# Kernel tuning notes

Measured on AMD Instinct MI355X. Metric: run time of the kernel, lower is better.

Reference implementation:

```python
import jax, jax.numpy as jnp
import numpy as np

B, NKV, NQ, D, H = 4, 2048, 1024, 1024, 16
HD = D // H


def setup_inputs() -> dict:
    key = jax.random.key(0)
    ks = jax.random.split(key, 9)
    s = 0.02
    return {
        "x": jax.random.normal(ks[0], (B, NKV, D), jnp.float32),
        "y": jax.random.normal(ks[1], (B, NQ, D), jnp.float32),
        "mask": jax.random.randint(ks[2], (B, NQ, NKV), 0, 2, jnp.int32),
        "W_kv": jax.random.normal(ks[3], (D, 2 * D), jnp.float32) * s,
        "b_kv": jnp.zeros((2 * D,), jnp.float32),
        "W_q": jax.random.normal(ks[4], (D, D), jnp.float32) * s,
        "b_q": jnp.zeros((D,), jnp.float32),
        "W_o": jax.random.normal(ks[5], (D, D), jnp.float32) * s,
        "b_o": jnp.zeros((D,), jnp.float32),
    }


def reference(x, y, mask, W_kv, b_kv, W_q, b_q, W_o, b_o):
    b, nkv, _ = x.shape
    nq = y.shape[1]
    kv = x @ W_kv + b_kv                                  # [B, NKV, 2D]
    q = y @ W_q + b_q                                     # [B, NQ, D]
    kv = kv.reshape(b, nkv, H, 2 * HD).transpose(0, 2, 1, 3)  # [B,H,NKV,2HD]
    q = q.reshape(b, nq, H, HD).transpose(0, 2, 1, 3)         # [B,H,NQ,HD]
    k, v = kv[..., :HD], kv[..., HD:]
    scores = jnp.einsum('bhqd,bhkd->bhqk', q, k) / jnp.sqrt(jnp.float32(HD))
    scores = jnp.where(mask[:, None, :, :] == 0, jnp.float32(-1e20), scores)
    attn = jax.nn.softmax(scores, axis=-1)
    vals = jnp.einsum('bhqk,bhkd->bhqd', attn, v)          # [B,H,NQ,HD]
    vals = vals.transpose(0, 2, 1, 3).reshape(b, nq, D)
    return vals @ W_o + b_o
```

## Files before the change

### kernel.cpp

```cpp
#include <hip/hip_runtime.h>
#include <hip/hip_bf16.h>
#include <math.h>

#define B_   4
#define NKV_ 2048
#define NQ_  1024
#define D_   1024
#define H_   16
#define HD_  64

typedef __attribute__((ext_vector_type(8))) short bf16x8;
typedef __attribute__((ext_vector_type(4))) float f32x4;

#define MFMA16x32(a, b, c) __builtin_amdgcn_mfma_f32_16x16x32_bf16((a), (b), (c), 0, 0, 0)

#define SC_LOG2 0.1803368801111244f

__device__ __forceinline__ short f2bf(float f) {
    unsigned u = __builtin_bit_cast(unsigned, f);
    u = (u + 0x7fff + ((u >> 16) & 1)) >> 16;
    return (short)u;
}
__device__ __forceinline__ unsigned cvt_pk_bf16(float lo, float hi) {
    unsigned r;
    asm("v_cvt_pk_bf16_f32 %0, %1, %2" : "=v"(r) : "v"(lo), "v"(hi));
    return r;
}
__device__ __forceinline__ void gload_lds16(const void* g, void* l) {
    __builtin_amdgcn_global_load_lds(
        (const __attribute__((address_space(1))) void*)g,
        (__attribute__((address_space(3))) void*)l, 16, 0, 0);
}
__device__ __forceinline__ void barrier_raw() {
    asm volatile("" ::: "memory");
    __builtin_amdgcn_s_barrier();
    asm volatile("" ::: "memory");
}

__global__ __launch_bounds__(256)
void prep(const float* __restrict__ Wkv, short* __restrict__ Tkv,
          const float* __restrict__ Wq,  short* __restrict__ Tq,
          const float* __restrict__ Wo,  short* __restrict__ To,
          const int* __restrict__ mask,  unsigned short* __restrict__ m16,
          const float* __restrict__ x,   short* __restrict__ xh, int n4x,
          const float* __restrict__ y,   short* __restrict__ yh, int n4y)
{
    const int bid = (int)blockIdx.x;
    if (bid < 4096) {
        const float* W; short* T; int K, N, bx, by;
        if (bid < 2048)      { W = Wkv; T = Tkv; K = D_; N = 2 * D_; bx = bid & 63;          by = bid >> 6; }
        else if (bid < 3072) { W = Wq;  T = Tq;  K = D_; N = D_;     bx = (bid - 2048) & 31; by = (bid - 2048) >> 5; }
        else                 { W = Wo;  T = To;  K = D_; N = D_;     bx = (bid - 3072) & 31; by = (bid - 3072) >> 5; }
        __shared__ float tile[32][33];
        const int tx = threadIdx.x & 31, ty = threadIdx.x >> 5;
        const int n0 = bx * 32, k0 = by * 32;
#pragma unroll
        for (int i = 0; i < 4; ++i)
            tile[ty + 8 * i][tx] = W[(size_t)(k0 + ty + 8 * i) * N + n0 + tx];
        __syncthreads();
#pragma unroll
        for (int i = 0; i < 4; ++i)
            T[(size_t)(n0 + ty + 8 * i) * K + k0 + tx] = f2bf(tile[tx][ty + 8 * i]);
    } else if (bid < 4608) {
        const int w = (bid - 4096) * 256 + threadIdx.x;
        const int4* pp = reinterpret_cast<const int4*>(mask + (size_t)w * 64);
        unsigned wg0 = 0, wg1 = 0, wg2 = 0, wg3 = 0;
#pragma unroll
        for (int i = 0; i < 16; ++i) {
            const int4 v = pp[i];
            const unsigned nib = (unsigned)(v.x != 0) | ((unsigned)(v.y != 0) << 1)
                               | ((unsigned)(v.z != 0) << 2) | ((unsigned)(v.w != 0) << 3);
            const unsigned sh = 4u * (unsigned)(i >> 2);
            if ((i & 3) == 0) wg0 |= nib << sh;
            else if ((i & 3) == 1) wg1 |= nib << sh;
            else if ((i & 3) == 2) wg2 |= nib << sh;
            else wg3 |= nib << sh;
        }
        ushort4 o;
        o.x = (unsigned short)wg0; o.y = (unsigned short)wg1;
        o.z = (unsigned short)wg2; o.w = (unsigned short)wg3;
        reinterpret_cast<ushort4*>(m16)[w] = o;
    } else {
        const int ntot = n4x + n4y;
        for (int i = (bid - 4608) * 256 + threadIdx.x; i < ntot; i += 2048 * 256) {
            const float4 v = (i < n4x)
                ? reinterpret_cast<const float4*>(x)[i]
                : reinterpret_cast<const float4*>(y)[i - n4x];
            short4 h;
            h.x = f2bf(v.x); h.y = f2bf(v.y); h.z = f2bf(v.z); h.w = f2bf(v.w);
            if (i < n4x) reinterpret_cast<short4*>(xh)[i] = h;
            else         reinterpret_cast<short4*>(yh)[i - n4x] = h;
        }
    }
}

__global__ __launch_bounds__(512, 2)
void proj256(const short* __restrict__ A, const short* __restrict__ Bm,
             const float* __restrict__ bias, short* __restrict__ Kout,
             short* __restrict__ Vtout)
{
    constexpr int K  = 1024;
    constexpr int NT = K / 32;
    constexpr int M  = B_ * NKV_;
    constexpr int N  = 2 * D_;

    __shared__ short At[4][8192];
    __shared__ short Bt[4][8192];

    const int t    = threadIdx.x;
    const int wave = t >> 6;
    const int lane = t & 63;
    const int fr   = lane & 15;
    const int kq   = lane >> 4;
    const int wm0  = (wave >> 2) * 128;
    const int wn0  = (wave & 3) * 64;

    const int gx  = N >> 8;
    const int gy  = M >> 8;
    const int lgx = __builtin_ctz(gx);
    const int bid = (int)blockIdx.x;
    const int xcd = bid & 7;
    const int j   = bid >> 3;
    const int m0  = (xcd * (gy >> 3) + (j >> lgx)) * 256;
    const int n0  = (j & (gx - 1)) * 256;

    const int r1 = t >> 2;
    const int g1 = (t & 3) ^ ((r1 >> 1) & 3);
    const int r2 = r1 + 128;

    f32x4 acc[8][4];
#pragma unroll
    for (int i = 0; i < 8; ++i)
#pragma unroll
        for (int j2 = 0; j2 < 4; ++j2) acc[i][j2] = f32x4{0.f, 0.f, 0.f, 0.f};

    auto stage = [&](int sb, int it) {
        const int kk = it << 5;
        gload_lds16(A  + (size_t)(m0 + r1) * K + kk + 8 * g1, &At[sb][wave * 512]);
        gload_lds16(A  + (size_t)(m0 + r2) * K + kk + 8 * g1, &At[sb][4096 + wave * 512]);
        gload_lds16(Bm + (size_t)(n0 + r1) * K + kk + 8 * g1, &Bt[sb][wave * 512]);
        gload_lds16(Bm + (size_t)(n0 + r2) * K + kk + 8 * g1, &Bt[sb][4096 + wave * 512]);
    };

    stage(0, 0);
    stage(1, 1);
    stage(2, 2);

    const int gsw = ((kq ^ ((fr >> 1) & 3)) << 3);
    for (int it = 0; it < NT; ++it) {
        if (it < NT - 2)       asm volatile("s_waitcnt vmcnt(8)" ::: "memory");
        else if (it == NT - 2) asm volatile("s_waitcnt vmcnt(4)" ::: "memory");
        else                   asm volatile("s_waitcnt vmcnt(0)" ::: "memory");
        barrier_raw();

        const int cb = it & 3;
        bf16x8 af[8], bf[4];
#pragma unroll
        for (int i = 0; i < 8; ++i)
            af[i] = *reinterpret_cast<const bf16x8*>(
                &At[cb][(wm0 + i * 16 + fr) * 32 + gsw]);
#pragma unroll
        for (int i = 0; i < 4; ++i)
            bf[i] = *reinterpret_cast<const bf16x8*>(
                &Bt[cb][(wn0 + i * 16 + fr) * 32 + gsw]);

        if (it + 3 < NT) stage((it + 3) & 3, it + 3);

        __builtin_amdgcn_s_setprio(1);
#pragma unroll
        for (int i = 0; i < 8; ++i)
#pragma unroll
            for (int j2 = 0; j2 < 4; ++j2)
                acc[i][j2] = MFMA16x32(af[i], bf[j2], acc[i][j2]);
        __builtin_amdgcn_s_setprio(0);
    }

#pragma unroll
    for (int i = 0; i < 8; ++i) {
#pragma unroll
        for (int j2 = 0; j2 < 4; ++j2) {
#pragma unroll
            for (int r = 0; r < 4; ++r) {
                const int m = m0 + wm0 + i * 16 + (lane >> 4) * 4 + r;
                const int n = n0 + wn0 + j2 * 16 + fr;
                const float v = acc[i][j2][r] + bias[n];
                const int b  = m >> 11;
                const int nk = m & 2047;
                const int h  = n >> 7;
                const int c  = n & 127;
                const int bh = b * H_ + h;
                if (c < 64)
                    Kout[(((size_t)bh * NKV_ + nk) << 6) + c] = f2bf(v);
                else
                    Vtout[((size_t)bh * 64 + (c - 64)) * NKV_ + nk] = f2bf(v);
            }
        }
    }
}

template<int MODE>
__global__ __launch_bounds__(256)
void gemm64(const short* __restrict__ Ahi, const short* __restrict__ Bhi,
            const float* __restrict__ bias, void* __restrict__ outv)
{
    __shared__ short At[3][2048];
    __shared__ short Bt[3][4096];

    const int M = B_ * NQ_, N = D_, K = D_;
    const int t    = threadIdx.x;
    const int wave = t >> 6;
    const int lane = t & 63;
    const int fr   = lane & 15;
    const int kq   = lane >> 4;

    const int gx  = N >> 7;
    const int gy  = M >> 6;
    const int lgx = __builtin_ctz(gx);
    const int bid = (int)blockIdx.x;
    const int xcd = bid & 7;
    const int j   = bid >> 3;
    const int m0  = (xcd * (gy >> 3) + (j >> lgx)) * 64;
    const int n0  = (j & (gx - 1)) * 128;

    const int wm0 = (wave & 1) * 32;
    const int wn0 = (wave >> 1) * 64;
    const int NT  = K >> 5;

    const int rA = t >> 2, gA = (t & 3) ^ ((rA >> 1) & 3);
    const int r1 = t >> 2,         g1 = (t & 3) ^ ((r1 >> 1) & 3);
    const int r2 = (t + 256) >> 2, g2 = (t & 3) ^ ((r2 >> 1) & 3);

    f32x4 acc[2][4];
#pragma unroll
    for (int i = 0; i < 2; ++i)
#pragma unroll
        for (int j2 = 0; j2 < 4; ++j2) acc[i][j2] = f32x4{0.f, 0.f, 0.f, 0.f};

    auto stage = [&](int sb, int it) {
        const int kk = it << 5;
        gload_lds16(Ahi + (size_t)(m0 + rA) * K + kk + 8 * gA, &At[sb][wave * 512]);
        gload_lds16(Bhi + (size_t)(n0 + r1) * K + kk + 8 * g1, &Bt[sb][wave * 512]);
        gload_lds16(Bhi + (size_t)(n0 + r2) * K + kk + 8 * g2, &Bt[sb][2048 + wave * 512]);
    };

    stage(0, 0);
    if (NT > 1) stage(1, 1);

    const int gsw = ((kq ^ ((fr >> 1) & 3)) << 3);
    for (int it = 0; it < NT; ++it) {
        if (it + 1 < NT) asm volatile("s_waitcnt vmcnt(3)" ::: "memory");
        else             asm volatile("s_waitcnt vmcnt(0)" ::: "memory");
        barrier_raw();

        const int cb = it % 3;
        bf16x8 af[2], bf[4];
#pragma unroll
        for (int i = 0; i < 2; ++i)
            af[i] = *reinterpret_cast<const bf16x8*>(&At[cb][(wm0 + i * 16 + fr) * 32 + gsw]);
#pragma unroll
        for (int i = 0; i < 4; ++i)
            bf[i] = *reinterpret_cast<const bf16x8*>(&Bt[cb][(wn0 + i * 16 + fr) * 32 + gsw]);
        if (it + 2 < NT) stage((it + 2) % 3, it + 2);

        __builtin_amdgcn_s_setprio(1);
#pragma unroll
        for (int i = 0; i < 2; ++i)
#pragma unroll
            for (int j2 = 0; j2 < 4; ++j2)
                acc[i][j2] = MFMA16x32(af[i], bf[j2], acc[i][j2]);
        __builtin_amdgcn_s_setprio(0);
    }

#pragma unroll
    for (int i = 0; i < 2; ++i)
#pragma unroll
        for (int j2 = 0; j2 < 4; ++j2)
#pragma unroll
            for (int r = 0; r < 4; ++r) {
                const int m = m0 + wm0 + i * 16 + (lane >> 4) * 4 + r;
                const int n = n0 + wn0 + j2 * 16 + fr;
                const float v = acc[i][j2][r] + bias[n];
                if (MODE == 1) {
                    short* Q_ = (short*)outv;
                    const int b = m >> 10;
                    const int q = m & 1023;
                    const int h = n >> 6;
                    const int d = n & 63;
                    Q_[(((size_t)(b * H_ + h) * NQ_ + q) << 6) + d] =
                        f2bf(v * SC_LOG2);
                } else {
                    ((float*)outv)[(size_t)m * N + n] = v;
                }
            }
}

__global__ __launch_bounds__(512)
void attn_mfma(const short* __restrict__ Q, const short* __restrict__ K,
               const short* __restrict__ Vt,
               const unsigned short* __restrict__ m16,
               float* __restrict__ Opart, float* __restrict__ Lpart)
{
    __shared__ short KtL[2][4096];
    __shared__ short VtL[2][4096];
    __shared__ short PsL[8192];

    const int t    = threadIdx.x;
    const int wave = t >> 6;
    const int lane = t & 63;
    const int fr   = lane & 15;
    const int g    = lane >> 4;

    const int bid = (int)blockIdx.x;
    const int xcd = bid & 7;
    const int j   = bid >> 3;
    const int bhl = j / 24;
    const int rem = j - bhl * 24;
    const int qt  = rem / 3;
    const int sp  = rem - qt * 3;
    const int bh  = xcd * 8 + bhl;
    const int b   = bh >> 4;
    const int h   = bh & 15;
    const int wq0 = qt * 128 + wave * 16;

    const int kts = sp * 11;
    const int kte = (sp == 2) ? 32 : kts + 11;

    const short* Kg  = K  + (size_t)bh * NKV_ * 64;
    const short* Vtg = Vt + (size_t)bh * 64 * NKV_;

    bf16x8 qf0, qf1;
    {
        const short* Qg = Q + ((size_t)bh * NQ_ + wq0 + fr) * 64 + g * 8;
        qf0 = *reinterpret_cast<const bf16x8*>(Qg);
        qf1 = *reinterpret_cast<const bf16x8*>(Qg + 32);
    }

    bf16x8 ones;
#pragma unroll
    for (int i = 0; i < 8; ++i) ones[i] = (short)0x3F80;

    f32x4 acc_o[4];
#pragma unroll
    for (int n = 0; n < 4; ++n) acc_o[n] = f32x4{0.f, 0.f, 0.f, 0.f};
    f32x4 lacc = f32x4{0.f, 0.f, 0.f, 0.f};

    const unsigned short* mbp =
        m16 + ((size_t)b * NQ_ + wq0 + fr) * (NKV_ / 64) * 4 + g;

    const int r8   = lane >> 3;
    const int csw  = ((lane & 7) << 3) ^ (r8 << 3);
    const int swzf = (fr & 7) << 3;
    short* PsW = PsL + wave * (16 * 64);

    auto stage = [&](int nb, int kt0) {
        const short* sK = Kg + (size_t)(kt0 + wave * 8 + r8) * 64 + csw;
        gload_lds16(sK, &KtL[nb][(wave * 8) * 64]);
        const short* sV = Vtg + (size_t)(wave * 8 + r8) * NKV_ + kt0 + csw;
        gload_lds16(sV, &VtL[nb][(wave * 8) * 64]);
    };

    stage(0, kts * 64);
    asm volatile("s_waitcnt vmcnt(0)" ::: "memory");
    __syncthreads();

    const int kcol0 = (8 * g) ^ swzf;
    const int kcol1 = (32 + 8 * g) ^ swzf;

    int cur = 0;
    for (int kt = kts; kt < kte; ++kt) {
        if (kt + 1 < kte) stage(cur ^ 1, (kt + 1) * 64);

        const unsigned mskv = mbp[(size_t)kt * 4];

        const short* KB = &KtL[cur][fr * 64];
        f32x4 s_acc[4];
        __builtin_amdgcn_s_setprio(1);
#pragma unroll
        for (int t4 = 0; t4 < 4; ++t4) {
            s_acc[t4] = f32x4{0.f, 0.f, 0.f, 0.f};
            const bf16x8 kf0 = *reinterpret_cast<const bf16x8*>(KB + t4 * 1024 + kcol0);
            const bf16x8 kf1 = *reinterpret_cast<const bf16x8*>(KB + t4 * 1024 + kcol1);
            s_acc[t4] = MFMA16x32(kf0, qf0, s_acc[t4]);
            s_acc[t4] = MFMA16x32(kf1, qf1, s_acc[t4]);
        }
        __builtin_amdgcn_s_setprio(0);

        float p[16];
#pragma unroll
        for (int t4 = 0; t4 < 4; ++t4)
#pragma unroll
            for (int r = 0; r < 4; ++r) {
                const int i = 4 * t4 + r;
                const float e = __builtin_amdgcn_exp2f(s_acc[t4][r]);
                p[i] = ((mskv >> i) & 1u) ? e : 0.f;
            }

#pragma unroll
        for (int t4 = 0; t4 < 4; ++t4) {
            uint2 w;
            w.x = cvt_pk_bf16(p[4 * t4 + 0], p[4 * t4 + 1]);
            w.y = cvt_pk_bf16(p[4 * t4 + 2], p[4 * t4 + 3]);
            *reinterpret_cast<uint2*>(&PsW[fr * 64 + ((16 * t4 + 4 * g) ^ swzf)]) = w;
        }

        {
            const bf16x8 pf0 = *reinterpret_cast<const bf16x8*>(&PsW[fr * 64 + kcol0]);
            const bf16x8 pf1 = *reinterpret_cast<const bf16x8*>(&PsW[fr * 64 + kcol1]);
            const short* VB = &VtL[cur][fr * 64];
            __builtin_amdgcn_s_setprio(1);
            lacc = MFMA16x32(ones, pf0, lacc);
            lacc = MFMA16x32(ones, pf1, lacc);
#pragma unroll
            for (int n = 0; n < 4; ++n) {
                const bf16x8 vf0 = *reinterpret_cast<const bf16x8*>(VB + n * 1024 + kcol0);
                const bf16x8 vf1 = *reinterpret_cast<const bf16x8*>(VB + n * 1024 + kcol1);
                acc_o[n] = MFMA16x32(vf0, pf0, acc_o[n]);
                acc_o[n] = MFMA16x32(vf1, pf1, acc_o[n]);
            }
            __builtin_amdgcn_s_setprio(0);
        }

        asm volatile("s_waitcnt vmcnt(0)" ::: "memory");
        __syncthreads();
        cur ^= 1;
    }

    float* Op = Opart + (size_t)sp * (B_ * NQ_ * D_);
    const size_t obase = ((size_t)b * NQ_ + wq0 + fr) * D_ + h * 64;
#pragma unroll
    for (int n = 0; n < 4; ++n) {
        float4 v;
        v.x = acc_o[n][0]; v.y = acc_o[n][1];
        v.z = acc_o[n][2]; v.w = acc_o[n][3];
        *reinterpret_cast<float4*>(&Op[obase + 16 * n + 4 * g]) = v;
    }
    if (g == 0)
        Lpart[(size_t)sp * (B_ * H_ * NQ_) + (size_t)bh * NQ_ + wq0 + fr] = lacc[0];
}

__global__ __launch_bounds__(256)
void combine(const float* __restrict__ Opart, const float* __restrict__ Lpart,
             short* __restrict__ valshi)
{
    const size_t npart = (size_t)B_ * NQ_ * D_;
    const size_t nl    = (size_t)B_ * H_ * NQ_;
    const int n4 = (int)(npart / 4);
    for (int i = blockIdx.x * 256 + threadIdx.x; i < n4; i += 2048 * 256) {
        const int row  = i >> 8;
        const int h    = (i & 255) >> 4;
        const int b    = row >> 10;
        const int q    = row & 1023;
        const float4 o0 = reinterpret_cast<const float4*>(Opart)[i];
        const float4 o1 = reinterpret_cast<const float4*>(Opart + npart)[i];
        const float4 o2 = reinterpret_cast<const float4*>(Opart + 2 * npart)[i];
        const size_t li = (size_t)(b * H_ + h) * NQ_ + q;
        const float inv = 1.f / (Lpart[li] + Lpart[nl + li] + Lpart[2 * nl + li]);
        short4 hh;
        hh.x = f2bf((o0.x + o1.x + o2.x) * inv);
        hh.y = f2bf((o0.y + o1.y + o2.y) * inv);
        hh.z = f2bf((o0.z + o1.z + o2.z) * inv);
        hh.w = f2bf((o0.w + o1.w + o2.w) * inv);
        reinterpret_cast<short4*>(valshi)[i] = hh;
    }
}

extern "C" void kernel_launch(void* const* d_in, const int* in_sizes, int n_in,
                              void* d_out, int out_size, void* d_ws, size_t ws_size,
                              hipStream_t stream)
{
    const float* x    = (const float*)d_in[0];
    const float* y    = (const float*)d_in[1];
    const int*   mask = (const int*)  d_in[2];
    const float* W_kv = (const float*)d_in[3];
    const float* b_kv = (const float*)d_in[4];
    const float* W_q  = (const float*)d_in[5];
    const float* b_q  = (const float*)d_in[6];
    const float* W_o  = (const float*)d_in[7];
    const float* b_o  = (const float*)d_in[8];
    float* out = (float*)d_out;

    char* p = (char*)d_ws;
    auto take = [&](size_t bytes) { char* r = p; p += bytes; return r; };
    short* xhi    = (short*)take((size_t)B_ * NKV_ * D_ * 2);
    short* yhi    = (short*)take((size_t)B_ * NQ_ * D_ * 2);
    short* Wkvthi = (short*)take((size_t)2 * D_ * D_ * 2);
    short* Wqthi  = (short*)take((size_t)D_ * D_ * 2);
    short* Wothi  = (short*)take((size_t)D_ * D_ * 2);
    short* Kbf    = (short*)take((size_t)B_ * H_ * NKV_ * HD_ * 2);
    short* Vtbf   = (short*)take((size_t)B_ * H_ * HD_ * NKV_ * 2);
    short* Qbf    = (short*)take((size_t)B_ * H_ * NQ_ * HD_ * 2);
    unsigned short* m16 =
        (unsigned short*)take((size_t)B_ * NQ_ * (NKV_ / 64) * 4 * 2);
    float* Opart  = (float*)take((size_t)3 * B_ * NQ_ * D_ * 4);
    float* Lpart  = (float*)take((size_t)3 * B_ * H_ * NQ_ * 4);
    short* valshi = xhi;

    prep<<<6656, 256, 0, stream>>>(W_kv, Wkvthi, W_q, Wqthi, W_o, Wothi,
                                   mask, m16,
                                   x, xhi, B_ * NKV_ * D_ / 4,
                                   y, yhi, B_ * NQ_ * D_ / 4);

    proj256<<<256, 512, 0, stream>>>(xhi, Wkvthi, b_kv, Kbf, Vtbf);

    gemm64<1><<<512, 256, 0, stream>>>(yhi, Wqthi, b_q, Qbf);

    attn_mfma<<<1536, 512, 0, stream>>>(Qbf, Kbf, Vtbf, m16, Opart, Lpart);

    combine<<<2048, 256, 0, stream>>>(Opart, Lpart, valshi);

    gemm64<2><<<512, 256, 0, stream>>>(valshi, Wothi, b_o, out);

    (void)in_sizes; (void)n_in; (void)out_size; (void)ws_size;
}
```

Before: 176.8 us.

## Drop split-KV attention with combine kernel; triple-buffer K/V with one barrier per tile

The attention kernel no longer splits the KV range three ways. Each of 512 blocks walks all 32 KV tiles and normalises and writes bf16 output directly, so the separate combine kernel and the fp32 partial buffers go away. Staging moves from double to triple buffering, with a counted vmcnt wait and a single raw barrier per iteration so loads run two tiles ahead. The trade is fewer blocks (512 instead of 1536) and therefore less parallelism across CUs, plus more LDS per block.

```diff
diff --git a/kernel.cpp b/kernel.cpp
--- a/kernel.cpp
+++ b/kernel.cpp
@@ -298,10 +298,10 @@
 void attn_mfma(const short* __restrict__ Q, const short* __restrict__ K,
                const short* __restrict__ Vt,
                const unsigned short* __restrict__ m16,
-               float* __restrict__ Opart, float* __restrict__ Lpart)
+               short* __restrict__ valshi)
 {
-    __shared__ short KtL[2][4096];
-    __shared__ short VtL[2][4096];
+    __shared__ short KtL[3][4096];
+    __shared__ short VtL[3][4096];
     __shared__ short PsL[8192];
 
     const int t    = threadIdx.x;
@@ -313,17 +313,10 @@
     const int bid = (int)blockIdx.x;
     const int xcd = bid & 7;
     const int j   = bid >> 3;
-    const int bhl = j / 24;
-    const int rem = j - bhl * 24;
-    const int qt  = rem / 3;
-    const int sp  = rem - qt * 3;
-    const int bh  = xcd * 8 + bhl;
+    const int bh  = xcd * 8 + (j >> 3);
     const int b   = bh >> 4;
     const int h   = bh & 15;
-    const int wq0 = qt * 128 + wave * 16;
-
-    const int kts = sp * 11;
-    const int kte = (sp == 2) ? 32 : kts + 11;
+    const int wq0 = (j & 7) * 128 + wave * 16;
 
     const short* Kg  = K  + (size_t)bh * NKV_ * 64;
     const short* Vtg = Vt + (size_t)bh * 64 * NKV_;
@@ -352,27 +345,31 @@
     const int swzf = (fr & 7) << 3;
     short* PsW = PsL + wave * (16 * 64);
 
-    auto stage = [&](int nb, int kt0) {
-        const short* sK = Kg + (size_t)(kt0 + wave * 8 + r8) * 64 + csw;
-        gload_lds16(sK, &KtL[nb][(wave * 8) * 64]);
-        const short* sV = Vtg + (size_t)(wave * 8 + r8) * NKV_ + kt0 + csw;
-        gload_lds16(sV, &VtL[nb][(wave * 8) * 64]);
+    auto stage = [&](int sb, int kt) {
+        const short* sK = Kg + (size_t)(kt * 64 + wave * 8 + r8) * 64 + csw;
+        gload_lds16(sK, &KtL[sb][(wave * 8) * 64]);
+        const short* sV = Vtg + (size_t)(wave * 8 + r8) * NKV_ + kt * 64 + csw;
+        gload_lds16(sV, &VtL[sb][(wave * 8) * 64]);
     };
 
-    stage(0, kts * 64);
-    asm volatile("s_waitcnt vmcnt(0)" ::: "memory");
-    __syncthreads();
+    constexpr int NTK = NKV_ / 64;
+    stage(0, 0);
+    stage(1, 1);
 
     const int kcol0 = (8 * g) ^ swzf;
     const int kcol1 = (32 + 8 * g) ^ swzf;
 
-    int cur = 0;
-    for (int kt = kts; kt < kte; ++kt) {
-        if (kt + 1 < kte) stage(cur ^ 1, (kt + 1) * 64);
+    for (int kt = 0; kt < NTK; ++kt) {
+        if (kt + 1 < NTK) asm volatile("s_waitcnt vmcnt(2)" ::: "memory");
+        else              asm volatile("s_waitcnt vmcnt(0)" ::: "memory");
+        barrier_raw();
+
+        const int cb = kt % 3;
+        if (kt + 2 < NTK) stage((kt + 2) % 3, kt + 2);
 
         const unsigned mskv = mbp[(size_t)kt * 4];
 
-        const short* KB = &KtL[cur][fr * 64];
+        const short* KB = &KtL[cb][fr * 64];
         f32x4 s_acc[4];
         __builtin_amdgcn_s_setprio(1);
 #pragma unroll
@@ -385,28 +382,26 @@
         }
         __builtin_amdgcn_s_setprio(0);
 
-        float p[16];
-#pragma unroll
-        for (int t4 = 0; t4 < 4; ++t4)
-#pragma unroll
-            for (int r = 0; r < 4; ++r) {
-                const int i = 4 * t4 + r;
-                const float e = __builtin_amdgcn_exp2f(s_acc[t4][r]);
-                p[i] = ((mskv >> i) & 1u) ? e : 0.f;
-            }
-
 #pragma unroll
         for (int t4 = 0; t4 < 4; ++t4) {
+            float e0 = __builtin_amdgcn_exp2f(s_acc[t4][0]);
+            float e1 = __builtin_amdgcn_exp2f(s_acc[t4][1]);
+            float e2 = __builtin_amdgcn_exp2f(s_acc[t4][2]);
+            float e3 = __builtin_amdgcn_exp2f(s_acc[t4][3]);
+            e0 = ((mskv >> (4 * t4 + 0)) & 1u) ? e0 : 0.f;
+            e1 = ((mskv >> (4 * t4 + 1)) & 1u) ? e1 : 0.f;
+            e2 = ((mskv >> (4 * t4 + 2)) & 1u) ? e2 : 0.f;
+            e3 = ((mskv >> (4 * t4 + 3)) & 1u) ? e3 : 0.f;
             uint2 w;
-            w.x = cvt_pk_bf16(p[4 * t4 + 0], p[4 * t4 + 1]);
-            w.y = cvt_pk_bf16(p[4 * t4 + 2], p[4 * t4 + 3]);
+            w.x = cvt_pk_bf16(e0, e1);
+            w.y = cvt_pk_bf16(e2, e3);
             *reinterpret_cast<uint2*>(&PsW[fr * 64 + ((16 * t4 + 4 * g) ^ swzf)]) = w;
         }
 
         {
             const bf16x8 pf0 = *reinterpret_cast<const bf16x8*>(&PsW[fr * 64 + kcol0]);
             const bf16x8 pf1 = *reinterpret_cast<const bf16x8*>(&PsW[fr * 64 + kcol1]);
-            const short* VB = &VtL[cur][fr * 64];
+            const short* VB = &VtL[cb][fr * 64];
             __builtin_amdgcn_s_setprio(1);
             lacc = MFMA16x32(ones, pf0, lacc);
             lacc = MFMA16x32(ones, pf1, lacc);
@@ -419,48 +414,18 @@
             }
             __builtin_amdgcn_s_setprio(0);
         }
-
-        asm volatile("s_waitcnt vmcnt(0)" ::: "memory");
-        __syncthreads();
-        cur ^= 1;
-    }
-
-    float* Op = Opart + (size_t)sp * (B_ * NQ_ * D_);
+    }
+
+    const float inv = 1.f / lacc[0];
     const size_t obase = ((size_t)b * NQ_ + wq0 + fr) * D_ + h * 64;
 #pragma unroll
     for (int n = 0; n < 4; ++n) {
-        float4 v;
-        v.x = acc_o[n][0]; v.y = acc_o[n][1];
-        v.z = acc_o[n][2]; v.w = acc_o[n][3];
-        *reinterpret_cast<float4*>(&Op[obase + 16 * n + 4 * g]) = v;
-    }
-    if (g == 0)
-        Lpart[(size_t)sp * (B_ * H_ * NQ_) + (size_t)bh * NQ_ + wq0 + fr] = lacc[0];
-}
-
-__global__ __launch_bounds__(256)
-void combine(const float* __restrict__ Opart, const float* __restrict__ Lpart,
-             short* __restrict__ valshi)
-{
-    const size_t npart = (size_t)B_ * NQ_ * D_;
-    const size_t nl    = (size_t)B_ * H_ * NQ_;
-    const int n4 = (int)(npart / 4);
-    for (int i = blockIdx.x * 256 + threadIdx.x; i < n4; i += 2048 * 256) {
-        const int row  = i >> 8;
-        const int h    = (i & 255) >> 4;
-        const int b    = row >> 10;
-        const int q    = row & 1023;
-        const float4 o0 = reinterpret_cast<const float4*>(Opart)[i];
-        const float4 o1 = reinterpret_cast<const float4*>(Opart + npart)[i];
-        const float4 o2 = reinterpret_cast<const float4*>(Opart + 2 * npart)[i];
-        const size_t li = (size_t)(b * H_ + h) * NQ_ + q;
-        const float inv = 1.f / (Lpart[li] + Lpart[nl + li] + Lpart[2 * nl + li]);
         short4 hh;
-        hh.x = f2bf((o0.x + o1.x + o2.x) * inv);
-        hh.y = f2bf((o0.y + o1.y + o2.y) * inv);
-        hh.z = f2bf((o0.z + o1.z + o2.z) * inv);
-        hh.w = f2bf((o0.w + o1.w + o2.w) * inv);
-        reinterpret_cast<short4*>(valshi)[i] = hh;
+        hh.x = f2bf(acc_o[n][0] * inv);
+        hh.y = f2bf(acc_o[n][1] * inv);
+        hh.z = f2bf(acc_o[n][2] * inv);
+        hh.w = f2bf(acc_o[n][3] * inv);
+        *reinterpret_cast<short4*>(&valshi[obase + 16 * n + 4 * g]) = hh;
     }
 }
 
@@ -491,8 +456,6 @@
     short* Qbf    = (short*)take((size_t)B_ * H_ * NQ_ * HD_ * 2);
     unsigned short* m16 =
         (unsigned short*)take((size_t)B_ * NQ_ * (NKV_ / 64) * 4 * 2);
-    float* Opart  = (float*)take((size_t)3 * B_ * NQ_ * D_ * 4);
-    float* Lpart  = (float*)take((size_t)3 * B_ * H_ * NQ_ * 4);
     short* valshi = xhi;
 
     prep<<<6656, 256, 0, stream>>>(W_kv, Wkvthi, W_q, Wqthi, W_o, Wothi,
@@ -504,9 +467,7 @@
 
     gemm64<1><<<512, 256, 0, stream>>>(yhi, Wqthi, b_q, Qbf);
 
-    attn_mfma<<<1536, 512, 0, stream>>>(Qbf, Kbf, Vtbf, m16, Opart, Lpart);
-
-    combine<<<2048, 256, 0, stream>>>(Opart, Lpart, valshi);
+    attn_mfma<<<512, 512, 0, stream>>>(Qbf, Kbf, Vtbf, m16, valshi);
 
     gemm64<2><<<512, 256, 0, stream>>>(valshi, Wothi, b_o, out);
 
```

Result: faster. 162.5 us (-8.1%).
